# Kernel tuning notes

Measured on AMD Instinct MI355X. Metric: run time of the kernel, lower is better.

Reference implementation:

```python
import jax, jax.numpy as jnp
import numpy as np

N_NODES = 10000
N_EDGES = 640000
IN_CH = 128
HID = 128
OUT = 2


def setup_inputs() -> dict:
    key = jax.random.key(0)
    ks = jax.random.split(key, 12)
    s_in = 1.0 / np.sqrt(IN_CH)
    s_2h = 1.0 / np.sqrt(2 * HID)
    s_h = 1.0 / np.sqrt(HID)
    return {
        "x": jax.random.normal(ks[0], (N_NODES, IN_CH), dtype=jnp.float32),
        "edge_index": jax.random.randint(ks[1], (2, N_EDGES), 0, N_NODES, dtype=jnp.int64),
        # SAGEConv: lin_l applied to aggregated neighbors (has bias), lin_r to self (no bias)
        "W_l": jax.random.uniform(ks[2], (IN_CH, HID), jnp.float32, -s_in, s_in),
        "b_l": jax.random.uniform(ks[3], (HID,), jnp.float32, -s_in, s_in),
        "W_r": jax.random.uniform(ks[4], (IN_CH, HID), jnp.float32, -s_in, s_in),
        # lin0: in -> hid
        "W0": jax.random.uniform(ks[5], (IN_CH, HID), jnp.float32, -s_in, s_in),
        "b0": jax.random.uniform(ks[6], (HID,), jnp.float32, -s_in, s_in),
        # lin1: 2*hid -> hid
        "W1": jax.random.uniform(ks[7], (2 * HID, HID), jnp.float32, -s_2h, s_2h),
        "b1": jax.random.uniform(ks[8], (HID,), jnp.float32, -s_2h, s_2h),
        # lin2: hid -> out
        "W2": jax.random.uniform(ks[9], (HID, OUT), jnp.float32, -s_h, s_h),
        "b2": jax.random.uniform(ks[10], (OUT,), jnp.float32, -s_h, s_h),
    }


def reference(x, edge_index, W_l, b_l, W_r, W0, b0, W1, b1, W2, b2):
    src, dst = edge_index[0], edge_index[1]
    # SAGE mean aggregation: gather source features, scatter-mean onto dst nodes
    msgs = x[src]                                                # [E, in]
    agg = jax.ops.segment_sum(msgs, dst, num_segments=N_NODES)  # [N, in]
    deg = jax.ops.segment_sum(jnp.ones((src.shape[0],), x.dtype), dst,
                              num_segments=N_NODES)              # [N]
    agg = agg / jnp.maximum(deg, 1.0)[:, None]
    # SAGEConv output: lin_l(agg) + lin_r(x)
    h = agg @ W_l + b_l + x @ W_r                                # [N, hid]
    h = jax.nn.relu(h)
    h = jnp.max(h, axis=-2)                                      # [hid] global max pool over nodes
    # concat branch: news node is x[0]
    news = jax.nn.relu(x[0] @ W0 + b0)                           # [hid]
    h = jax.nn.relu(jnp.concatenate([news, h], axis=-1) @ W1 + b1)
    return h @ W2 + b2                                           # [out]
```

## Files before the change

### kernel.cpp

```cpp
#include <hip/hip_runtime.h>
#include <hip/hip_bf16.h>

#define NCH 128
#define NPART 64
#define NRANGE 512
#define SEGCAP 48
#define RCAP 2560
#define PSMAX 32

typedef __attribute__((ext_vector_type(8))) short bfrag;
typedef __attribute__((ext_vector_type(4))) float ffrag;

__device__ inline unsigned int f2bf_pair(float lo, float hi) {
    unsigned int ul = __float_as_uint(lo);
    unsigned int uh = __float_as_uint(hi);
    ul = (ul + 0x7fffu + ((ul >> 16) & 1u)) >> 16;
    uh = (uh + 0x7fffu + ((uh >> 16) & 1u)) & 0xffff0000u;
    return (ul & 0xffffu) | uh;
}

__global__ __launch_bounds__(256) void k_partprep(
    const float2* __restrict__ x2, const float* __restrict__ Wl,
    const float* __restrict__ Wr, const int* __restrict__ ei32,
    const long long* __restrict__ ei64, unsigned int* __restrict__ M32,
    unsigned int* __restrict__ Wt32, unsigned int* __restrict__ seg,
    int* __restrict__ segcnt, int n2, int N, int E, int PSr) {
    const int t = threadIdx.x;
    if (blockIdx.x < NPART) {
        __shared__ int sflag;
        __shared__ int cur[NRANGE];
        if (t < 64) {
            int v = ei32[2 * t + 1];
            unsigned long long b = __ballot(v != 0);
            if (t == 0) sflag = (b == 0ULL) ? 1 : 0;
        }
        for (int i = t; i < NRANGE; i += 256) cur[i] = 0;
        __syncthreads();
        const int flag = sflag;
        const int b = blockIdx.x;
        const int ES = (E + NPART - 1) / NPART;
        const int e0 = b * ES, e1 = min(E, e0 + ES);
        for (int e = e0 + t; e < e1; e += 256) {
            int src, dst;
            if (flag) { src = (int)ei64[e]; dst = (int)ei64[(size_t)E + e]; }
            else      { src = ei32[e];      dst = ei32[(size_t)E + e]; }
            int r = dst / PSr;
            int dl = dst - r * PSr;
            int pos = atomicAdd(&cur[r], 1);
            if (pos < SEGCAP)
                seg[((size_t)b * NRANGE + r) * SEGCAP + pos] =
                    ((unsigned int)dl << 16) | (unsigned int)src;
        }
        __syncthreads();
        for (int i = t; i < NRANGE; i += 256)
            segcnt[b * NRANGE + i] = min(cur[i], SEGCAP);
        return;
    }
    int i = (int)(blockIdx.x - NPART) * 256 + t;
    if (i < n2) {
        float2 v = x2[i];
        int n = i >> 6, c = i & 63;
        M32[n * 128 + 64 + c] = f2bf_pair(v.x, v.y);
        return;
    }
    int j = i - n2;
    if (j < 128 * 128) {
        int c = j & 127, kp = j >> 7;
        int k0 = 2 * kp, k1 = 2 * kp + 1;
        float v0 = (k0 < 128) ? Wl[k0 * 128 + c] : Wr[(k0 - 128) * 128 + c];
        float v1 = (k1 < 128) ? Wl[k1 * 128 + c] : Wr[(k1 - 128) * 128 + c];
        Wt32[c * 128 + kp] = f2bf_pair(v0, v1);
    }
}

__global__ __launch_bounds__(512) void k_aggdense(
    const unsigned int* __restrict__ seg, const int* __restrict__ segcnt,
    const unsigned int* __restrict__ M32, const short* __restrict__ Wt,
    const float* __restrict__ bl, unsigned int* __restrict__ hmaxU,
    int N, int PSr) {
    __shared__ unsigned int tmp[RCAP];
    __shared__ unsigned short scsr[RCAP];
    __shared__ unsigned int aggL[PSMAX * 66];
    __shared__ int sc[NPART];
    __shared__ int hist[PSMAX], startp[PSMAX], cur[PSMAX];
    __shared__ float red[8][32];
    const int r = blockIdx.x;
    const int t = threadIdx.x;

    if (t < NPART) sc[t] = segcnt[t * NRANGE + r];
    for (int i = t; i < PSMAX * 66; i += 512) aggL[i] = 0;
    if (t < PSMAX) hist[t] = 0;
    __syncthreads();
    for (int off = 1; off < NPART; off <<= 1) {
        int v = (t >= off && t < NPART) ? sc[t - off] : 0;
        __syncthreads();
        if (t < NPART) sc[t] += v;
        __syncthreads();
    }
    const int total = min(sc[NPART - 1], RCAP);

    for (int i = t; i < total; i += 512) {
        int lo = 0, hi = NPART - 1;
        while (lo < hi) { int mid = (lo + hi) >> 1; if (sc[mid] > i) hi = mid; else lo = mid + 1; }
        int excl = (lo == 0) ? 0 : sc[lo - 1];
        tmp[i] = seg[((size_t)lo * NRANGE + r) * SEGCAP + (i - excl)];
    }
    __syncthreads();
    for (int i = t; i < total; i += 512) atomicAdd(&hist[tmp[i] >> 16], 1);
    __syncthreads();
    if (t == 0) {
        int run = 0;
        for (int i = 0; i < PSMAX; ++i) { startp[i] = run; cur[i] = run; run += hist[i]; }
    }
    __syncthreads();
    for (int i = t; i < total; i += 512) {
        unsigned int v = tmp[i];
        int pos = atomicAdd(&cur[v >> 16], 1);
        scsr[pos] = (unsigned short)(v & 0xffffu);
    }
    __syncthreads();

    const int wave = t >> 6, lane = t & 63;
    for (int li = wave; li < PSr; li += 8) {
        int node = r * PSr + li;
        if (node >= N) break;
        int base = startp[li], d = hist[li];
        float ax = 0.f, ay = 0.f;
        int i = 0;
        for (; i + 8 <= d; i += 8) {
            int s[8];
            unsigned int u[8];
#pragma unroll
            for (int j = 0; j < 8; ++j) s[j] = scsr[base + i + j];
#pragma unroll
            for (int j = 0; j < 8; ++j) u[j] = M32[s[j] * 128 + 64 + lane];
#pragma unroll
            for (int j = 0; j < 8; ++j) {
                ax += __uint_as_float(u[j] << 16);
                ay += __uint_as_float(u[j] & 0xffff0000u);
            }
        }
        for (; i < d; ++i) {
            unsigned int u = M32[((int)scsr[base + i]) * 128 + 64 + lane];
            ax += __uint_as_float(u << 16);
            ay += __uint_as_float(u & 0xffff0000u);
        }
        float sca = 1.0f / fmaxf((float)d, 1.0f);
        aggL[li * 66 + lane] = f2bf_pair(ax * sca, ay * sca);
    }
    __syncthreads();

    const int l16 = lane & 15, quad = lane >> 4;
    const int rt = wave & 1, cg = wave >> 1;
    const int lrow = rt * 16 + l16;
    bfrag a[8];
#pragma unroll
    for (int kk = 0; kk < 4; ++kk)
        a[kk] = *(const bfrag*)((const short*)(aggL + lrow * 66 + kk * 16 + quad * 4));
    {
        int mc = min(r * PSr + lrow, N - 1);
#pragma unroll
        for (int kk = 0; kk < 4; ++kk)
            a[4 + kk] = *(const bfrag*)((const short*)(M32 + (size_t)mc * 128 + 64)
                                        + kk * 32 + quad * 8);
    }
    float mx[2];
#pragma unroll
    for (int ct = 0; ct < 2; ++ct) {
        int col = cg * 32 + ct * 16 + l16;
        float bv = bl[col];
        ffrag acc = {bv, bv, bv, bv};
        const short* wp = Wt + (size_t)col * 256 + quad * 8;
#pragma unroll
        for (int kk = 0; kk < 8; ++kk) {
            bfrag b = *(const bfrag*)(wp + kk * 32);
            acc = __builtin_amdgcn_mfma_f32_16x16x32_bf16(a[kk], b, acc, 0, 0, 0);
        }
        float lm = 0.f;
#pragma unroll
        for (int rr = 0; rr < 4; ++rr) {
            int lr = rt * 16 + quad * 4 + rr;
            int nd = r * PSr + lr;
            if (lr < PSr && nd < N) lm = fmaxf(lm, fmaxf(acc[rr], 0.f));
        }
        lm = fmaxf(lm, __shfl_xor(lm, 16));
        lm = fmaxf(lm, __shfl_xor(lm, 32));
        mx[ct] = lm;
    }
    if (lane < 16) {
        red[wave][l16]      = mx[0];
        red[wave][16 + l16] = mx[1];
    }
    __syncthreads();
    if (t < 128) {
        int cg2 = t >> 5, wi = t & 31;
        float v = fmaxf(red[2 * cg2][wi], red[2 * cg2 + 1][wi]);
        atomicMax(&hmaxU[t], __float_as_uint(v));
    }
}

__global__ __launch_bounds__(1024) void k_head(
    const float* __restrict__ x, const float* __restrict__ hmax,
    const float* __restrict__ W0, const float* __restrict__ b0,
    const float* __restrict__ W1, const float* __restrict__ b1,
    const float* __restrict__ W2, const float* __restrict__ b2,
    float* __restrict__ out) {
    __shared__ float xs[NCH];
    __shared__ float part[8][NCH];
    __shared__ float cat[2 * NCH];
    __shared__ float h1[NCH];
    __shared__ float pr[2][NCH];
    const int t = threadIdx.x;
    const int c = t & 127, seg = t >> 7;
    if (t < NCH) xs[t] = x[t];
    __syncthreads();
    {
        float a0 = 0.f, a1 = 0.f, a2 = 0.f, a3 = 0.f;
        int k0 = seg * 16;
#pragma unroll
        for (int j = 0; j < 16; j += 4) {
            a0 += xs[k0 + j + 0] * W0[(k0 + j + 0) * NCH + c];
            a1 += xs[k0 + j + 1] * W0[(k0 + j + 1) * NCH + c];
            a2 += xs[k0 + j + 2] * W0[(k0 + j + 2) * NCH + c];
            a3 += xs[k0 + j + 3] * W0[(k0 + j + 3) * NCH + c];
        }
        part[seg][c] = (a0 + a1) + (a2 + a3);
    }
    __syncthreads();
    if (t < NCH) {
        float s = b0[t];
#pragma unroll
        for (int g = 0; g < 8; ++g) s += part[g][t];
        cat[t] = fmaxf(s, 0.f);
        cat[NCH + t] = hmax[t];
    }
    __syncthreads();
    {
        float a0 = 0.f, a1 = 0.f, a2 = 0.f, a3 = 0.f;
        int k0 = seg * 32;
#pragma unroll
        for (int j = 0; j < 32; j += 4) {
            a0 += cat[k0 + j + 0] * W1[(k0 + j + 0) * NCH + c];
            a1 += cat[k0 + j + 1] * W1[(k0 + j + 1) * NCH + c];
            a2 += cat[k0 + j + 2] * W1[(k0 + j + 2) * NCH + c];
            a3 += cat[k0 + j + 3] * W1[(k0 + j + 3) * NCH + c];
        }
        part[seg][c] = (a0 + a1) + (a2 + a3);
    }
    __syncthreads();
    if (t < NCH) {
        float s = b1[t];
#pragma unroll
        for (int g = 0; g < 8; ++g) s += part[g][t];
        h1[t] = fmaxf(s, 0.f);
    }
    __syncthreads();
    if (t < NCH) {
        float2 w = ((const float2*)W2)[t];
        pr[0][t] = h1[t] * w.x;
        pr[1][t] = h1[t] * w.y;
    }
    __syncthreads();
    for (int off = 64; off >= 1; off >>= 1) {
        if (t < off) { pr[0][t] += pr[0][t + off]; pr[1][t] += pr[1][t + off]; }
        __syncthreads();
    }
    if (t < 2) out[t] = pr[t][0] + b2[t];
}

__global__ void k_detect(const int* __restrict__ ei, int* __restrict__ flag) {
    int v = ei[2 * threadIdx.x + 1];
    unsigned long long b = __ballot(v != 0);
    if (threadIdx.x == 0) *flag = (b == 0ULL) ? 1 : 0;
}
__global__ void k_hist(const int* __restrict__ ei32, const long long* __restrict__ ei64,
                       const int* __restrict__ flag, int* __restrict__ cnt, int E) {
    int e = blockIdx.x * blockDim.x + threadIdx.x;
    if (e >= E) return;
    int dst = (*flag) ? (int)ei64[(size_t)E + e] : ei32[(size_t)E + e];
    atomicAdd(&cnt[dst], 1);
}
__global__ void k_scan(const int* __restrict__ cnt, int* __restrict__ row_start, int N) {
    __shared__ int lds[1024];
    int t = threadIdx.x;
    int chunk = (N + 1023) / 1024;
    int base = t * chunk;
    int sum = 0;
    for (int i = 0; i < chunk; ++i) {
        int idx = base + i;
        if (idx < N) sum += cnt[idx];
    }
    lds[t] = sum;
    __syncthreads();
    for (int off = 1; off < 1024; off <<= 1) {
        int v = (t >= off) ? lds[t - off] : 0;
        __syncthreads();
        lds[t] += v;
        __syncthreads();
    }
    int run = (t == 0) ? 0 : lds[t - 1];
    for (int i = 0; i < chunk; ++i) {
        int idx = base + i;
        if (idx < N) { row_start[idx] = run; run += cnt[idx]; }
    }
    if (t == 1023) row_start[N] = run;
}
__global__ void k_fill(const int* __restrict__ ei32, const long long* __restrict__ ei64,
                       const int* __restrict__ flag, const int* __restrict__ row_start,
                       int* __restrict__ cursor, int* __restrict__ csr, int E) {
    int e = blockIdx.x * blockDim.x + threadIdx.x;
    if (e >= E) return;
    int src, dst;
    if (*flag) { src = (int)ei64[e]; dst = (int)ei64[(size_t)E + e]; }
    else       { src = ei32[e];      dst = ei32[(size_t)E + e]; }
    int pos = atomicAdd(&cursor[dst], 1);
    csr[row_start[dst] + pos] = src;
}
__global__ __launch_bounds__(256) void k_agg_linmax(
    const float* __restrict__ x, const int* __restrict__ row_start,
    const int* __restrict__ csr, const float* __restrict__ Wl,
    const float* __restrict__ bl, const float* __restrict__ Wr,
    unsigned int* __restrict__ hmaxU, int N, int E) {
    const int lane = threadIdx.x & 63;
    const int wave = threadIdx.x >> 6;
    const int group = blockIdx.x * 4 + wave;
    const int ngroups = (N + 3) / 4;
    const float2* __restrict__ x2  = (const float2*)x;
    const float2* __restrict__ Wl2 = (const float2*)Wl;
    const float2* __restrict__ Wr2 = (const float2*)Wr;
    const float2* __restrict__ bl2 = (const float2*)bl;
    float2 m = make_float2(0.f, 0.f);
    if (group < ngroups) {
        int n0 = group * 4;
        int s[4], d[4];
#pragma unroll
        for (int q = 0; q < 4; ++q) {
            int n = n0 + q;
            if (n < N) { s[q] = row_start[n]; d[q] = row_start[n + 1] - s[q]; }
            else       { s[q] = 0; d[q] = 0; }
        }
        int maxd = max(max(d[0], d[1]), max(d[2], d[3]));
        float2 acc[4];
#pragma unroll
        for (int q = 0; q < 4; ++q) acc[q] = make_float2(0.f, 0.f);
        int idxv[4] = {0, 0, 0, 0};
        for (int i = 0; i < maxd; ++i) {
            int t = i & 63;
            if (t == 0) {
#pragma unroll
                for (int q = 0; q < 4; ++q) {
                    if (i < d[q]) {
                        int a = s[q] + i + lane;
                        a = (a < E) ? a : (E - 1);
                        idxv[q] = csr[a];
                    }
                }
            }
#pragma unroll
            for (int q = 0; q < 4; ++q) {
                if (i < d[q]) {
                    int src = __shfl(idxv[q], t);
                    float2 v = x2[src * 64 + lane];
                    acc[q].x += v.x; acc[q].y += v.y;
                }
            }
        }
        float2 xv[4];
#pragma unroll
        for (int q = 0; q < 4; ++q) {
            float sc = 1.0f / fmaxf((float)d[q], 1.0f);
            acc[q].x *= sc; acc[q].y *= sc;
            int n = n0 + q;
            xv[q] = (n < N) ? x2[n * 64 + lane] : make_float2(0.f, 0.f);
        }
        float2 o[4];
#pragma unroll
        for (int q = 0; q < 4; ++q) o[q] = bl2[lane];
        for (int j = 0; j < 64; ++j) {
            float2 wl0 = Wl2[(2 * j) * 64 + lane];
            float2 wl1 = Wl2[(2 * j + 1) * 64 + lane];
            float2 wr0 = Wr2[(2 * j) * 64 + lane];
            float2 wr1 = Wr2[(2 * j + 1) * 64 + lane];
#pragma unroll
            for (int q = 0; q < 4; ++q) {
                float ax = __shfl(acc[q].x, j);
                float ay = __shfl(acc[q].y, j);
                float xx = __shfl(xv[q].x, j);
                float xy = __shfl(xv[q].y, j);
                o[q].x += ax * wl0.x + ay * wl1.x + xx * wr0.x + xy * wr1.x;
                o[q].y += ax * wl0.y + ay * wl1.y + xx * wr0.y + xy * wr1.y;
            }
        }
#pragma unroll
        for (int q = 0; q < 4; ++q) {
            if (n0 + q < N) {
                m.x = fmaxf(m.x, fmaxf(o[q].x, 0.f));
                m.y = fmaxf(m.y, fmaxf(o[q].y, 0.f));
            }
        }
    }
    __shared__ float2 red2[4][64];
    red2[wave][lane] = m;
    __syncthreads();
    if (wave == 0) {
#pragma unroll
        for (int ww = 1; ww < 4; ++ww) {
            m.x = fmaxf(m.x, red2[ww][lane].x);
            m.y = fmaxf(m.y, red2[ww][lane].y);
        }
        atomicMax(&hmaxU[2 * lane],     __float_as_uint(m.x));
        atomicMax(&hmaxU[2 * lane + 1], __float_as_uint(m.y));
    }
}
__global__ void k_head_fb(const float* __restrict__ x, const float* __restrict__ hmax,
                          const float* __restrict__ W0, const float* __restrict__ b0,
                          const float* __restrict__ W1, const float* __restrict__ b1,
                          const float* __restrict__ W2, const float* __restrict__ b2,
                          float* __restrict__ out) {
    __shared__ float s_cat[2 * NCH];
    __shared__ float s_part[256];
    __shared__ float s_h1[NCH];
    int t = threadIdx.x;
    if (t < NCH) {
        float acc = b0[t];
        for (int k = 0; k < NCH; ++k) acc += x[k] * W0[k * NCH + t];
        s_cat[t] = fmaxf(acc, 0.f);
        s_cat[NCH + t] = hmax[t];
    }
    __syncthreads();
    {
        int c = t & 127, half = t >> 7;
        float p = 0.f;
        int k0 = half * NCH;
        for (int k = k0; k < k0 + NCH; ++k) p += s_cat[k] * W1[k * NCH + c];
        s_part[t] = p;
    }
    __syncthreads();
    if (t < NCH) s_h1[t] = fmaxf(s_part[t] + s_part[NCH + t] + b1[t], 0.f);
    __syncthreads();
    if (t < 2) {
        float o = b2[t];
        for (int k = 0; k < NCH; ++k) o += s_h1[k] * W2[k * 2 + t];
        out[t] = o;
    }
}

extern "C" void kernel_launch(void* const* d_in, const int* in_sizes, int n_in,
                              void* d_out, int out_size, void* d_ws, size_t ws_size,
                              hipStream_t stream) {
    const float* x  = (const float*)d_in[0];
    const void*  ei = d_in[1];
    const float* Wl = (const float*)d_in[2];
    const float* bl = (const float*)d_in[3];
    const float* Wr = (const float*)d_in[4];
    const float* W0 = (const float*)d_in[5];
    const float* b0 = (const float*)d_in[6];
    const float* W1 = (const float*)d_in[7];
    const float* b1 = (const float*)d_in[8];
    const float* W2 = (const float*)d_in[9];
    const float* b2 = (const float*)d_in[10];
    float* out = (float*)d_out;

    const int N = in_sizes[0] / NCH;
    const int E = in_sizes[1] / 2;
    const int n2 = N * 64;
    const int PSr = (N + NRANGE - 1) / NRANGE;

    int* iws = (int*)d_ws;
    unsigned int* hmaxU = (unsigned int*)iws;
    int* segcnt = iws + 128;
    unsigned int* seg = (unsigned int*)(segcnt + NPART * NRANGE);
    unsigned int* Wt32 = seg + (size_t)NPART * NRANGE * SEGCAP;
    unsigned int* M32  = Wt32 + 128 * 128;
    size_t need = ((size_t)128 + NPART * NRANGE +
                   (size_t)NPART * NRANGE * SEGCAP + 128 * 128 +
                   (size_t)N * 128) * 4;
    bool main_ok = (need <= ws_size) && (N <= NRANGE * PSMAX) && (N <= 65535) &&
                   (PSr >= 1);

    if (main_ok) {
        hipMemsetAsync(d_ws, 0, 512, stream);
        int prepb = (n2 + 128 * 128 + 255) / 256;
        k_partprep<<<NPART + prepb, 256, 0, stream>>>(
            (const float2*)x, Wl, Wr, (const int*)ei, (const long long*)ei,
            M32, Wt32, seg, segcnt, n2, N, E, PSr);
        k_aggdense<<<NRANGE, 512, 0, stream>>>(seg, segcnt, M32, (const short*)Wt32,
                                               bl, hmaxU, N, PSr);
        k_head<<<1, 1024, 0, stream>>>(x, (const float*)hmaxU, W0, b0, W1, b1, W2, b2, out);
        return;
    }

    int* fcnt      = iws;
    int* fcursor   = iws + N;
    unsigned int* fhmax = (unsigned int*)(iws + 2 * N);
    int* flag      = iws + 2 * N + 128;
    int* frs       = iws + 2 * N + 132;
    int* fcsr      = iws + 3 * N + 144;

    hipMemsetAsync(d_ws, 0, (size_t)(2 * N + 128) * sizeof(int), stream);
    k_detect<<<1, 64, 0, stream>>>((const int*)ei, flag);
    k_hist<<<(E + 255) / 256, 256, 0, stream>>>((const int*)ei, (const long long*)ei,
                                                flag, fcnt, E);
    k_scan<<<1, 1024, 0, stream>>>(fcnt, frs, N);
    k_fill<<<(E + 255) / 256, 256, 0, stream>>>((const int*)ei, (const long long*)ei,
                                                flag, frs, fcursor, fcsr, E);
    int ngroups = (N + 3) / 4;
    k_agg_linmax<<<(ngroups + 3) / 4, 256, 0, stream>>>(x, frs, fcsr, Wl, bl, Wr,
                                                        fhmax, N, E);
    k_head_fb<<<1, 256, 0, stream>>>(x, (const float*)fhmax, W0, b0, W1, b1, W2, b2, out);
}
```

Measured before the change: 138.9 us.

## Fuse head MLP into aggregation kernel via last-block pattern, drop memset

```diff
diff --git a/kernel.cpp b/kernel.cpp
--- a/kernel.cpp
+++ b/kernel.cpp
@@ -2,9 +2,9 @@
 #include <hip/hip_bf16.h>
 
 #define NCH 128
-#define NPART 64
+#define NPART 128
 #define NRANGE 512
-#define SEGCAP 48
+#define SEGCAP 32
 #define RCAP 2560
 #define PSMAX 32
 
@@ -24,9 +24,14 @@
     const float* __restrict__ Wr, const int* __restrict__ ei32,
     const long long* __restrict__ ei64, unsigned int* __restrict__ M32,
     unsigned int* __restrict__ Wt32, unsigned int* __restrict__ seg,
-    int* __restrict__ segcnt, int n2, int N, int E, int PSr) {
+    int* __restrict__ segcnt, unsigned int* __restrict__ hmaxU,
+    int* __restrict__ done, int n2, int N, int E, int PSr) {
     const int t = threadIdx.x;
     if (blockIdx.x < NPART) {
+        if (blockIdx.x == 0) {
+            if (t < 128) hmaxU[t] = 0u;
+            if (t == 128) *done = 0;
+        }
         __shared__ int sflag;
         __shared__ int cur[NRANGE];
         if (t < 64) {
@@ -77,13 +82,18 @@
     const unsigned int* __restrict__ seg, const int* __restrict__ segcnt,
     const unsigned int* __restrict__ M32, const short* __restrict__ Wt,
     const float* __restrict__ bl, unsigned int* __restrict__ hmaxU,
-    int N, int PSr) {
+    int* __restrict__ done, const float* __restrict__ x,
+    const float* __restrict__ W0, const float* __restrict__ b0,
+    const float* __restrict__ W1, const float* __restrict__ b1,
+    const float* __restrict__ W2, const float* __restrict__ b2,
+    float* __restrict__ out, int N, int PSr) {
     __shared__ unsigned int tmp[RCAP];
     __shared__ unsigned short scsr[RCAP];
     __shared__ unsigned int aggL[PSMAX * 66];
     __shared__ int sc[NPART];
     __shared__ int hist[PSMAX], startp[PSMAX], cur[PSMAX];
     __shared__ float red[8][32];
+    __shared__ int lastflag;
     const int r = blockIdx.x;
     const int t = threadIdx.x;
 
@@ -127,6 +137,19 @@
         int base = startp[li], d = hist[li];
         float ax = 0.f, ay = 0.f;
         int i = 0;
+        for (; i + 16 <= d; i += 16) {
+            int s[16];
+            unsigned int u[16];
+#pragma unroll
+            for (int j = 0; j < 16; ++j) s[j] = scsr[base + i + j];
+#pragma unroll
+            for (int j = 0; j < 16; ++j) u[j] = M32[s[j] * 128 + 64 + lane];
+#pragma unroll
+            for (int j = 0; j < 16; ++j) {
+                ax += __uint_as_float(u[j] << 16);
+                ay += __uint_as_float(u[j] & 0xffff0000u);
+            }
+        }
         for (; i + 8 <= d; i += 8) {
             int s[8];
             unsigned int u[8];
@@ -197,75 +220,73 @@
         float v = fmaxf(red[2 * cg2][wi], red[2 * cg2 + 1][wi]);
         atomicMax(&hmaxU[t], __float_as_uint(v));
     }
-}
-
-__global__ __launch_bounds__(1024) void k_head(
-    const float* __restrict__ x, const float* __restrict__ hmax,
-    const float* __restrict__ W0, const float* __restrict__ b0,
-    const float* __restrict__ W1, const float* __restrict__ b1,
-    const float* __restrict__ W2, const float* __restrict__ b2,
-    float* __restrict__ out) {
-    __shared__ float xs[NCH];
-    __shared__ float part[8][NCH];
-    __shared__ float cat[2 * NCH];
-    __shared__ float h1[NCH];
-    __shared__ float pr[2][NCH];
-    const int t = threadIdx.x;
-    const int c = t & 127, seg = t >> 7;
-    if (t < NCH) xs[t] = x[t];
+
+    __syncthreads();
+    if (t == 0) {
+        __threadfence();
+        int old = atomicAdd(done, 1);
+        lastflag = (old == NRANGE - 1) ? 1 : 0;
+    }
+    __syncthreads();
+    if (!lastflag) return;
+    __threadfence();
+
+    float* hs   = (float*)tmp;
+    float* cat  = hs;
+    float* part = hs + 256;
+    float* h1p  = hs + 768;
+    float* pr   = hs + 896;
+    float* xsp  = hs + 1152;
+    const int c = t & 127, sg = t >> 7;
+    if (t < 128) {
+        xsp[t] = x[t];
+        cat[128 + t] = __uint_as_float(atomicOr(&hmaxU[t], 0u));
+    }
     __syncthreads();
     {
         float a0 = 0.f, a1 = 0.f, a2 = 0.f, a3 = 0.f;
-        int k0 = seg * 16;
-#pragma unroll
-        for (int j = 0; j < 16; j += 4) {
-            a0 += xs[k0 + j + 0] * W0[(k0 + j + 0) * NCH + c];
-            a1 += xs[k0 + j + 1] * W0[(k0 + j + 1) * NCH + c];
-            a2 += xs[k0 + j + 2] * W0[(k0 + j + 2) * NCH + c];
-            a3 += xs[k0 + j + 3] * W0[(k0 + j + 3) * NCH + c];
-        }
-        part[seg][c] = (a0 + a1) + (a2 + a3);
-    }
-    __syncthreads();
-    if (t < NCH) {
-        float s = b0[t];
-#pragma unroll
-        for (int g = 0; g < 8; ++g) s += part[g][t];
-        cat[t] = fmaxf(s, 0.f);
-        cat[NCH + t] = hmax[t];
-    }
+        int k0 = sg * 32;
+#pragma unroll
+        for (int j = 0; j < 32; j += 4) {
+            a0 += xsp[k0 + j + 0] * W0[(k0 + j + 0) * NCH + c];
+            a1 += xsp[k0 + j + 1] * W0[(k0 + j + 1) * NCH + c];
+            a2 += xsp[k0 + j + 2] * W0[(k0 + j + 2) * NCH + c];
+            a3 += xsp[k0 + j + 3] * W0[(k0 + j + 3) * NCH + c];
+        }
+        part[sg * 128 + c] = (a0 + a1) + (a2 + a3);
+    }
+    __syncthreads();
+    if (t < 128)
+        cat[t] = fmaxf(b0[t] + part[t] + part[128 + t] + part[256 + t] + part[384 + t], 0.f);
     __syncthreads();
     {
         float a0 = 0.f, a1 = 0.f, a2 = 0.f, a3 = 0.f;
-        int k0 = seg * 32;
-#pragma unroll
-        for (int j = 0; j < 32; j += 4) {
+        int k0 = sg * 64;
+#pragma unroll
+        for (int j = 0; j < 64; j += 4) {
             a0 += cat[k0 + j + 0] * W1[(k0 + j + 0) * NCH + c];
             a1 += cat[k0 + j + 1] * W1[(k0 + j + 1) * NCH + c];
             a2 += cat[k0 + j + 2] * W1[(k0 + j + 2) * NCH + c];
             a3 += cat[k0 + j + 3] * W1[(k0 + j + 3) * NCH + c];
         }
-        part[seg][c] = (a0 + a1) + (a2 + a3);
-    }
-    __syncthreads();
-    if (t < NCH) {
-        float s = b1[t];
-#pragma unroll
-        for (int g = 0; g < 8; ++g) s += part[g][t];
-        h1[t] = fmaxf(s, 0.f);
-    }
-    __syncthreads();
-    if (t < NCH) {
+        part[sg * 128 + c] = (a0 + a1) + (a2 + a3);
+    }
+    __syncthreads();
+    if (t < 128)
+        h1p[t] = fmaxf(b1[t] + part[t] + part[128 + t] + part[256 + t] + part[384 + t], 0.f);
+    __syncthreads();
+    if (t < 128) {
         float2 w = ((const float2*)W2)[t];
-        pr[0][t] = h1[t] * w.x;
-        pr[1][t] = h1[t] * w.y;
+        pr[t]       = h1p[t] * w.x;
+        pr[128 + t] = h1p[t] * w.y;
     }
     __syncthreads();
     for (int off = 64; off >= 1; off >>= 1) {
-        if (t < off) { pr[0][t] += pr[0][t + off]; pr[1][t] += pr[1][t + off]; }
-        __syncthreads();
-    }
-    if (t < 2) out[t] = pr[t][0] + b2[t];
+        if (t < off) { pr[t] += pr[t + off]; pr[128 + t] += pr[128 + t + off]; }
+        __syncthreads();
+    }
+    if (t == 0) out[0] = pr[0] + b2[0];
+    if (t == 1) out[1] = pr[128] + b2[1];
 }
 
 __global__ void k_detect(const int* __restrict__ ei, int* __restrict__ flag) {
@@ -468,25 +489,25 @@
 
     int* iws = (int*)d_ws;
     unsigned int* hmaxU = (unsigned int*)iws;
-    int* segcnt = iws + 128;
+    int* done = iws + 128;
+    int* segcnt = iws + 192;
     unsigned int* seg = (unsigned int*)(segcnt + NPART * NRANGE);
     unsigned int* Wt32 = seg + (size_t)NPART * NRANGE * SEGCAP;
     unsigned int* M32  = Wt32 + 128 * 128;
-    size_t need = ((size_t)128 + NPART * NRANGE +
+    size_t need = ((size_t)192 + NPART * NRANGE +
                    (size_t)NPART * NRANGE * SEGCAP + 128 * 128 +
                    (size_t)N * 128) * 4;
     bool main_ok = (need <= ws_size) && (N <= NRANGE * PSMAX) && (N <= 65535) &&
-                   (PSr >= 1);
+                   (PSr >= 1) && (PSr <= PSMAX);
 
     if (main_ok) {
-        hipMemsetAsync(d_ws, 0, 512, stream);
         int prepb = (n2 + 128 * 128 + 255) / 256;
         k_partprep<<<NPART + prepb, 256, 0, stream>>>(
             (const float2*)x, Wl, Wr, (const int*)ei, (const long long*)ei,
-            M32, Wt32, seg, segcnt, n2, N, E, PSr);
+            M32, Wt32, seg, segcnt, hmaxU, done, n2, N, E, PSr);
         k_aggdense<<<NRANGE, 512, 0, stream>>>(seg, segcnt, M32, (const short*)Wt32,
-                                               bl, hmaxU, N, PSr);
-        k_head<<<1, 1024, 0, stream>>>(x, (const float*)hmaxU, W0, b0, W1, b1, W2, b2, out);
+                                               bl, hmaxU, done, x,
+                                               W0, b0, W1, b1, W2, b2, out, N, PSr);
         return;
     }
 
```

Result: faster. 130.7 us (-5.9%).
